# Optimization experiments

Hardware: AMD Instinct MI355X
Metric: run time of the kernel (lower is better)

## Reference

```python
import jax, jax.numpy as jnp
import numpy as np

N_NODES = 100000
N_EDGES = 1600000
IN_DIM = 128
HID = 32
HEADS = 4
OUT_DIM = 40
BN_EPS = 1e-5
NEG_SLOPE = 0.2


def _gat_conv(x, src, dst, W, att_src, att_dst, bias, concat):
    # x: [N, F_in]; src/dst: [E] (self-loops already appended)
    H, C = att_src.shape
    h = (x @ W).reshape(-1, H, C)                       # [N, H, C]
    a_s = jnp.sum(h * att_src, axis=-1)                 # [N, H]
    a_d = jnp.sum(h * att_dst, axis=-1)                 # [N, H]
    e = jax.nn.leaky_relu(a_s[src] + a_d[dst], NEG_SLOPE)  # [E, H]
    # segment softmax over incoming edges of each destination node
    m = jax.ops.segment_max(e, dst, num_segments=N_NODES)
    m = jnp.where(jnp.isfinite(m), m, 0.0)
    p = jnp.exp(e - m[dst])
    denom = jax.ops.segment_sum(p, dst, num_segments=N_NODES)
    alpha = p / (denom[dst] + 1e-16)                    # [E, H]
    out = jax.ops.segment_sum(h[src] * alpha[..., None], dst, num_segments=N_NODES)  # [N, H, C]
    out = out.reshape(N_NODES, H * C) if concat else out.mean(axis=1)
    return out + bias


def _bn_eval(x, gamma, beta, rm, rv):
    return (x - rm) * jax.lax.rsqrt(rv + BN_EPS) * gamma + beta


def setup_inputs() -> dict:
    key = jax.random.key(0)
    ks = jax.random.split(key, 16)
    d = {}
    d["x"] = jax.random.normal(ks[0], (N_NODES, IN_DIM), dtype=jnp.float32)
    d["edge_index"] = jax.random.randint(ks[1], (2, N_EDGES), 0, N_NODES, dtype=jnp.int64 if jax.config.jax_enable_x64 else jnp.int32)
    s = 0.1
    # conv1: IN_DIM -> HID x HEADS (concat)
    d["W1"] = jax.random.normal(ks[2], (IN_DIM, HEADS * HID), jnp.float32) * s
    d["as1"] = jax.random.normal(ks[3], (HEADS, HID), jnp.float32) * s
    d["ad1"] = jax.random.normal(ks[4], (HEADS, HID), jnp.float32) * s
    d["b1"] = jnp.zeros((HEADS * HID,), jnp.float32)
    d["g1"] = jnp.ones((HEADS * HID,), jnp.float32)
    d["beta1"] = jnp.zeros((HEADS * HID,), jnp.float32)
    d["rm1"] = jnp.zeros((HEADS * HID,), jnp.float32)
    d["rv1"] = jnp.ones((HEADS * HID,), jnp.float32)
    # conv2: HID*HEADS -> HID (1 head, no concat)
    d["W2"] = jax.random.normal(ks[5], (HEADS * HID, HID), jnp.float32) * s
    d["as2"] = jax.random.normal(ks[6], (1, HID), jnp.float32) * s
    d["ad2"] = jax.random.normal(ks[7], (1, HID), jnp.float32) * s
    d["b2"] = jnp.zeros((HID,), jnp.float32)
    d["g2"] = jnp.ones((HID,), jnp.float32)
    d["beta2"] = jnp.zeros((HID,), jnp.float32)
    d["rm2"] = jnp.zeros((HID,), jnp.float32)
    d["rv2"] = jnp.ones((HID,), jnp.float32)
    # conv3: HID -> OUT_DIM (1 head, no concat)
    d["W3"] = jax.random.normal(ks[8], (HID, OUT_DIM), jnp.float32) * s
    d["as3"] = jax.random.normal(ks[9], (1, OUT_DIM), jnp.float32) * s
    d["ad3"] = jax.random.normal(ks[10], (1, OUT_DIM), jnp.float32) * s
    d["b3"] = jnp.zeros((OUT_DIM,), jnp.float32)
    return d


def reference(x, edge_index, W1, as1, ad1, b1, g1, beta1, rm1, rv1,
              W2, as2, ad2, b2, g2, beta2, rm2, rv2, W3, as3, ad3, b3):
    # add self-loops (PyG GATConv default), shared by all three layers
    loops = jnp.arange(N_NODES, dtype=edge_index.dtype)
    src = jnp.concatenate([edge_index[0], loops])
    dst = jnp.concatenate([edge_index[1], loops])
    h = _gat_conv(x, src, dst, W1, as1, ad1, b1, concat=True)
    h = jax.nn.elu(_bn_eval(h, g1, beta1, rm1, rv1))
    h = _gat_conv(h, src, dst, W2, as2, ad2, b2, concat=False)
    h = jax.nn.elu(_bn_eval(h, g2, beta2, rm2, rv2))
    out = _gat_conv(h, src, dst, W3, as3, ad3, b3, concat=False)
    return jax.nn.log_softmax(out, axis=1)
```

## Files before the change

### kernel.cpp

```cpp
#include <hip/hip_runtime.h>
#include <math.h>

#define N_NODES 100000
#define N_EDGES 1600000
#define E_TOT   (N_EDGES + N_NODES)
#define BN_EPS  1e-5f
#define NEG_SLOPE 0.2f
#define NINF (-INFINITY)


__global__ __launch_bounds__(256) void k_count(const int* __restrict__ ei,
                                               int* __restrict__ cnt) {
    int i = blockIdx.x * blockDim.x + threadIdx.x;
    if (i >= E_TOT) return;
    int d = (i < N_EDGES) ? ei[N_EDGES + i] : (i - N_EDGES);
    atomicAdd(&cnt[d], 1);
}

__global__ __launch_bounds__(256) void k_scan1(const int* __restrict__ cnt,
                                               int* __restrict__ excl,
                                               int* __restrict__ sums) {
    __shared__ int lds[256];
    int t = threadIdx.x;
    int base = blockIdx.x * 1024 + t * 4;
    int a[4];
#pragma unroll
    for (int j = 0; j < 4; ++j) a[j] = (base + j < N_NODES) ? cnt[base + j] : 0;
    int tot = a[0] + a[1] + a[2] + a[3];
    lds[t] = tot;
    __syncthreads();
    for (int off = 1; off < 256; off <<= 1) {
        int v = (t >= off) ? lds[t - off] : 0;
        __syncthreads();
        lds[t] += v;
        __syncthreads();
    }
    int run = lds[t] - tot;
#pragma unroll
    for (int j = 0; j < 4; ++j) {
        if (base + j < N_NODES) excl[base + j] = run;
        run += a[j];
    }
    if (t == 255) sums[blockIdx.x] = lds[255];
}

__global__ void k_scan2(int* sums, int nb) {
    if (blockIdx.x == 0 && threadIdx.x == 0) {
        int run = 0;
        for (int i = 0; i < nb; ++i) { int v = sums[i]; sums[i] = run; run += v; }
    }
}

__global__ __launch_bounds__(256) void k_scan3(int* __restrict__ row_ptr,
                                               int* __restrict__ cursor,
                                               const int* __restrict__ sums) {
    int i = blockIdx.x * blockDim.x + threadIdx.x;
    if (i == 0) row_ptr[N_NODES] = E_TOT;
    if (i >= N_NODES) return;
    int v = row_ptr[i] + sums[i >> 10];
    row_ptr[i] = v;
    cursor[i] = v;
}

__global__ __launch_bounds__(256) void k_scatter(const int* __restrict__ ei,
                                                 int* __restrict__ cursor,
                                                 int* __restrict__ col_idx) {
    int i = blockIdx.x * blockDim.x + threadIdx.x;
    if (i >= E_TOT) return;
    int s, d;
    if (i < N_EDGES) { s = ei[i]; d = ei[N_EDGES + i]; }
    else             { s = d = i - N_EDGES; }
    int pos = atomicAdd(&cursor[d], 1);
    col_idx[pos] = s;
}


template <int K, int NC, int BM, int BLOCK>
__global__ __launch_bounds__(BLOCK) void k_gemm(const float* __restrict__ X,
                                                const float* __restrict__ W,
                                                float* __restrict__ Hout,
                                                int nrows) {
    constexpr int CG  = NC / 4;
    constexpr int TR  = BLOCK / CG;
    constexpr int RPT = BM / TR;
    constexpr int LDK = K + 4;
    __shared__ float xs[BM * LDK];
    const int row0 = blockIdx.x * BM;
    const int vr = (nrows - row0 < BM) ? (nrows - row0) : BM;
    const int nvalid = vr * K;
    for (int i = threadIdx.x * 4; i < BM * K; i += BLOCK * 4) {
        float4 v = make_float4(0.f, 0.f, 0.f, 0.f);
        if (i < nvalid) v = *(const float4*)(X + (size_t)row0 * K + i);
        int row = i / K, col = i % K;
        *(float4*)(&xs[row * LDK + col]) = v;
    }
    __syncthreads();
    const int tx = threadIdx.x % CG;
    const int ty = threadIdx.x / CG;
    float4 acc[RPT];
#pragma unroll
    for (int r = 0; r < RPT; ++r) acc[r] = make_float4(0.f, 0.f, 0.f, 0.f);
    for (int k4 = 0; k4 < K / 4; ++k4) {
        const float4 w0 = *(const float4*)(W + (k4 * 4 + 0) * NC + tx * 4);
        const float4 w1 = *(const float4*)(W + (k4 * 4 + 1) * NC + tx * 4);
        const float4 w2 = *(const float4*)(W + (k4 * 4 + 2) * NC + tx * 4);
        const float4 w3 = *(const float4*)(W + (k4 * 4 + 3) * NC + tx * 4);
#pragma unroll
        for (int r = 0; r < RPT; ++r) {
            const float4 xv = *(const float4*)(&xs[(ty * RPT + r) * LDK + k4 * 4]);
            acc[r].x = fmaf(xv.w, w3.x, fmaf(xv.z, w2.x, fmaf(xv.y, w1.x, fmaf(xv.x, w0.x, acc[r].x))));
            acc[r].y = fmaf(xv.w, w3.y, fmaf(xv.z, w2.y, fmaf(xv.y, w1.y, fmaf(xv.x, w0.y, acc[r].y))));
            acc[r].z = fmaf(xv.w, w3.z, fmaf(xv.z, w2.z, fmaf(xv.y, w1.z, fmaf(xv.x, w0.z, acc[r].z))));
            acc[r].w = fmaf(xv.w, w3.w, fmaf(xv.z, w2.w, fmaf(xv.y, w1.w, fmaf(xv.x, w0.w, acc[r].w))));
        }
    }
#pragma unroll
    for (int r = 0; r < RPT; ++r) {
        int row = row0 + ty * RPT + r;
        if (row < nrows) *(float4*)(Hout + (size_t)row * NC + tx * 4) = acc[r];
    }
}


__global__ __launch_bounds__(256) void k_attproj1(const float* __restrict__ h,
                                                  const float* __restrict__ asf,
                                                  const float* __restrict__ adf,
                                                  float* __restrict__ a_s,
                                                  float* __restrict__ a_d) {
    int wv = (blockIdx.x * blockDim.x + threadIdx.x) >> 6;
    int lane = threadIdx.x & 63;
    if (wv >= N_NODES) return;
    float hlo = h[(size_t)wv * 128 + lane];
    float hhi = h[(size_t)wv * 128 + 64 + lane];
    float s0 = hlo * asf[lane], s1 = hhi * asf[64 + lane];
    float d0 = hlo * adf[lane], d1 = hhi * adf[64 + lane];
#pragma unroll
    for (int off = 1; off < 32; off <<= 1) {
        s0 += __shfl_xor(s0, off); s1 += __shfl_xor(s1, off);
        d0 += __shfl_xor(d0, off); d1 += __shfl_xor(d1, off);
    }
    if (lane == 0)  { a_s[wv * 4 + 0] = s0; a_s[wv * 4 + 2] = s1;
                      a_d[wv * 4 + 0] = d0; a_d[wv * 4 + 2] = d1; }
    if (lane == 32) { a_s[wv * 4 + 1] = s0; a_s[wv * 4 + 3] = s1;
                      a_d[wv * 4 + 1] = d0; a_d[wv * 4 + 3] = d1; }
}

__global__ __launch_bounds__(256) void k_attproj2(const float* __restrict__ h,
                                                  const float* __restrict__ asf,
                                                  const float* __restrict__ adf,
                                                  float* __restrict__ a_s,
                                                  float* __restrict__ a_d) {
    int wv = (blockIdx.x * blockDim.x + threadIdx.x) >> 6;
    int lane = threadIdx.x & 63;
    if (wv * 2 >= N_NODES) return;
    int n = wv * 2 + (lane >> 5);
    int l = lane & 31;
    float hv = h[(size_t)n * 32 + l];
    float s = hv * asf[l], d = hv * adf[l];
#pragma unroll
    for (int off = 1; off < 32; off <<= 1) { s += __shfl_xor(s, off); d += __shfl_xor(d, off); }
    if (l == 0) { a_s[n] = s; a_d[n] = d; }
}

__global__ __launch_bounds__(256) void k_attproj3(const float* __restrict__ h,
                                                  const float* __restrict__ asf,
                                                  const float* __restrict__ adf,
                                                  float* __restrict__ a_s,
                                                  float* __restrict__ a_d) {
    int wv = (blockIdx.x * blockDim.x + threadIdx.x) >> 6;
    int lane = threadIdx.x & 63;
    if (wv >= N_NODES) return;
    float hv = (lane < 40) ? h[(size_t)wv * 40 + lane] : 0.f;
    float s = (lane < 40) ? hv * asf[lane] : 0.f;
    float d = (lane < 40) ? hv * adf[lane] : 0.f;
#pragma unroll
    for (int off = 1; off < 64; off <<= 1) { s += __shfl_xor(s, off); d += __shfl_xor(d, off); }
    if (lane == 0) { a_s[wv] = s; a_d[wv] = d; }
}


__global__ __launch_bounds__(256) void k_agg1(const float* __restrict__ h,
                                              const float* __restrict__ a_s,
                                              const float* __restrict__ a_d,
                                              const int* __restrict__ row_ptr,
                                              const int* __restrict__ col_idx,
                                              const float* __restrict__ b,
                                              const float* __restrict__ g,
                                              const float* __restrict__ beta,
                                              const float* __restrict__ rm,
                                              const float* __restrict__ rv,
                                              float* __restrict__ obuf) {
    __shared__ float4 lp[4 * 64];
    __shared__ int    lc[4 * 64];
    const int wid  = threadIdx.x >> 6;
    const int lane = threadIdx.x & 63;
    const int n = (blockIdx.x << 2) + wid;
    if (n >= N_NODES) return;
    float4* lpw = lp + (wid << 6);
    int*    lcw = lc + (wid << 6);
    const int hi = lane >> 5;
    const float4 ad4 = *(const float4*)(a_d + (size_t)n * 4);
    const int beg = row_ptr[n], end = row_ptr[n + 1];
    const int deg = end - beg;
    float den0 = 0.f, den1 = 0.f, den2 = 0.f, den3 = 0.f;
    float acc0 = 0.f, acc1 = 0.f;

    if (deg <= 64) {
        const int idx = beg + lane;
        const bool v = idx < end;
        const int col = v ? col_idx[idx] : 0;
        float e0, e1, e2, e3;
        if (v) {
            float4 as4 = *(const float4*)(a_s + (size_t)col * 4);
            e0 = as4.x + ad4.x; e0 = e0 > 0.f ? e0 : NEG_SLOPE * e0;
            e1 = as4.y + ad4.y; e1 = e1 > 0.f ? e1 : NEG_SLOPE * e1;
            e2 = as4.z + ad4.z; e2 = e2 > 0.f ? e2 : NEG_SLOPE * e2;
            e3 = as4.w + ad4.w; e3 = e3 > 0.f ? e3 : NEG_SLOPE * e3;
        } else { e0 = e1 = e2 = e3 = NINF; }
        float m0 = e0, m1 = e1, m2 = e2, m3 = e3;
#pragma unroll
        for (int off = 1; off < 64; off <<= 1) {
            m0 = fmaxf(m0, __shfl_xor(m0, off));
            m1 = fmaxf(m1, __shfl_xor(m1, off));
            m2 = fmaxf(m2, __shfl_xor(m2, off));
            m3 = fmaxf(m3, __shfl_xor(m3, off));
        }
        float p0 = __expf(e0 - m0), p1 = __expf(e1 - m1);
        float p2 = __expf(e2 - m2), p3 = __expf(e3 - m3);
        lpw[lane] = make_float4(p0, p1, p2, p3);
        lcw[lane] = col;
        den0 = p0; den1 = p1; den2 = p2; den3 = p3;
#pragma unroll
        for (int off = 1; off < 64; off <<= 1) {
            den0 += __shfl_xor(den0, off); den1 += __shfl_xor(den1, off);
            den2 += __shfl_xor(den2, off); den3 += __shfl_xor(den3, off);
        }
        const int cnt = (deg + 1) & ~1;
        for (int j = 0; j < cnt; j += 2) {
            float4 pa = lpw[j];
            float4 pb = lpw[j + 1];
            int c0 = lcw[j], c1 = lcw[j + 1];
            const float* r0 = h + (size_t)c0 * 128;
            const float* r1 = h + (size_t)c1 * 128;
            float h00 = r0[lane], h01 = r0[64 + lane];
            float h10 = r1[lane], h11 = r1[64 + lane];
            float pA0 = hi ? pa.y : pa.x, pB0 = hi ? pa.w : pa.z;
            float pA1 = hi ? pb.y : pb.x, pB1 = hi ? pb.w : pb.z;
            acc0 += pA0 * h00 + pA1 * h10;
            acc1 += pB0 * h01 + pB1 * h11;
        }
    } else {
        float m0 = NINF, m1 = NINF, m2 = NINF, m3 = NINF;
        for (int c = beg; c < end; c += 64) {
            int idx = c + lane;
            bool v = idx < end;
            if (v) {
                int col = col_idx[idx];
                float4 as4 = *(const float4*)(a_s + (size_t)col * 4);
                float e0 = as4.x + ad4.x; e0 = e0 > 0.f ? e0 : NEG_SLOPE * e0;
                float e1 = as4.y + ad4.y; e1 = e1 > 0.f ? e1 : NEG_SLOPE * e1;
                float e2 = as4.z + ad4.z; e2 = e2 > 0.f ? e2 : NEG_SLOPE * e2;
                float e3 = as4.w + ad4.w; e3 = e3 > 0.f ? e3 : NEG_SLOPE * e3;
                m0 = fmaxf(m0, e0); m1 = fmaxf(m1, e1);
                m2 = fmaxf(m2, e2); m3 = fmaxf(m3, e3);
            }
        }
#pragma unroll
        for (int off = 1; off < 64; off <<= 1) {
            m0 = fmaxf(m0, __shfl_xor(m0, off));
            m1 = fmaxf(m1, __shfl_xor(m1, off));
            m2 = fmaxf(m2, __shfl_xor(m2, off));
            m3 = fmaxf(m3, __shfl_xor(m3, off));
        }
        for (int c = beg; c < end; c += 64) {
            int idx = c + lane;
            bool v = idx < end;
            int col = v ? col_idx[idx] : 0;
            float p0 = 0.f, p1 = 0.f, p2 = 0.f, p3 = 0.f;
            if (v) {
                float4 as4 = *(const float4*)(a_s + (size_t)col * 4);
                float e0 = as4.x + ad4.x; e0 = e0 > 0.f ? e0 : NEG_SLOPE * e0;
                float e1 = as4.y + ad4.y; e1 = e1 > 0.f ? e1 : NEG_SLOPE * e1;
                float e2 = as4.z + ad4.z; e2 = e2 > 0.f ? e2 : NEG_SLOPE * e2;
                float e3 = as4.w + ad4.w; e3 = e3 > 0.f ? e3 : NEG_SLOPE * e3;
                p0 = __expf(e0 - m0); p1 = __expf(e1 - m1);
                p2 = __expf(e2 - m2); p3 = __expf(e3 - m3);
            }
            lpw[lane] = make_float4(p0, p1, p2, p3);
            lcw[lane] = col;
            float s0 = p0, s1 = p1, s2 = p2, s3 = p3;
#pragma unroll
            for (int off = 1; off < 64; off <<= 1) {
                s0 += __shfl_xor(s0, off); s1 += __shfl_xor(s1, off);
                s2 += __shfl_xor(s2, off); s3 += __shfl_xor(s3, off);
            }
            den0 += s0; den1 += s1; den2 += s2; den3 += s3;
            int csz = end - c; if (csz > 64) csz = 64;
            int cnt = (csz + 1) & ~1;
            for (int j = 0; j < cnt; j += 2) {
                float4 pa = lpw[j];
                float4 pb = lpw[j + 1];
                int c0i = lcw[j], c1i = lcw[j + 1];
                const float* r0 = h + (size_t)c0i * 128;
                const float* r1 = h + (size_t)c1i * 128;
                float h00 = r0[lane], h01 = r0[64 + lane];
                float h10 = r1[lane], h11 = r1[64 + lane];
                float pA0 = hi ? pa.y : pa.x, pB0 = hi ? pa.w : pa.z;
                float pA1 = hi ? pb.y : pb.x, pB1 = hi ? pb.w : pb.z;
                acc0 += pA0 * h00 + pA1 * h10;
                acc1 += pB0 * h01 + pB1 * h11;
            }
        }
    }

    float inv0 = 1.f / (den0 + 1e-16f), inv1 = 1.f / (den1 + 1e-16f);
    float inv2 = 1.f / (den2 + 1e-16f), inv3 = 1.f / (den3 + 1e-16f);
    float f0 = acc0 * (hi ? inv1 : inv0);
    float f1 = acc1 * (hi ? inv3 : inv2);
    int fA = lane, fB = lane + 64;
    f0 += b[fA]; f1 += b[fB];
    f0 = (f0 - rm[fA]) * rsqrtf(rv[fA] + BN_EPS) * g[fA] + beta[fA];
    f1 = (f1 - rm[fB]) * rsqrtf(rv[fB] + BN_EPS) * g[fB] + beta[fB];
    f0 = f0 > 0.f ? f0 : (__expf(f0) - 1.f);
    f1 = f1 > 0.f ? f1 : (__expf(f1) - 1.f);
    obuf[(size_t)n * 128 + fA] = f0;
    obuf[(size_t)n * 128 + fB] = f1;
}

__global__ __launch_bounds__(256) void k_agg2(const float* __restrict__ h,
                                              const float* __restrict__ a_s,
                                              const float* __restrict__ a_d,
                                              const int* __restrict__ row_ptr,
                                              const int* __restrict__ col_idx,
                                              const float* __restrict__ b,
                                              const float* __restrict__ g,
                                              const float* __restrict__ beta,
                                              const float* __restrict__ rm,
                                              const float* __restrict__ rv,
                                              float* __restrict__ obuf) {
    __shared__ float lp[4 * 64];
    __shared__ int   lc[4 * 64];
    const int wid  = threadIdx.x >> 6;
    const int lane = threadIdx.x & 63;
    const int n = (blockIdx.x << 2) + wid;
    if (n >= N_NODES) return;
    float* lpw = lp + (wid << 6);
    int*   lcw = lc + (wid << 6);
    const int l31 = lane & 31, hh = lane >> 5;
    const float ad = a_d[n];
    const int beg = row_ptr[n], end = row_ptr[n + 1];
    const int deg = end - beg;
    float den = 0.f, acc = 0.f;

    if (deg <= 64) {
        const int idx = beg + lane;
        const bool v = idx < end;
        const int col = v ? col_idx[idx] : 0;
        float e = NINF;
        if (v) {
            e = a_s[col] + ad;
            e = e > 0.f ? e : NEG_SLOPE * e;
        }
        float m = e;
#pragma unroll
        for (int off = 1; off < 64; off <<= 1) m = fmaxf(m, __shfl_xor(m, off));
        float p = __expf(e - m);
        lpw[lane] = p;
        lcw[lane] = col;
        den = p;
#pragma unroll
        for (int off = 1; off < 64; off <<= 1) den += __shfl_xor(den, off);
        const int cnt = (deg + 1) & ~1;
        for (int j = 0; j < cnt; j += 2) {
            int jj = j + hh;
            float p_ = lpw[jj];
            int c  = lcw[jj];
            acc += p_ * h[(size_t)c * 32 + l31];
        }
    } else {
        float m = NINF;
        for (int c = beg; c < end; c += 64) {
            int idx = c + lane;
            if (idx < end) {
                float e = a_s[col_idx[idx]] + ad;
                e = e > 0.f ? e : NEG_SLOPE * e;
                m = fmaxf(m, e);
            }
        }
#pragma unroll
        for (int off = 1; off < 64; off <<= 1) m = fmaxf(m, __shfl_xor(m, off));
        for (int c = beg; c < end; c += 64) {
            int idx = c + lane;
            bool v = idx < end;
            int col = v ? col_idx[idx] : 0;
            float p = 0.f;
            if (v) {
                float e = a_s[col] + ad;
                e = e > 0.f ? e : NEG_SLOPE * e;
                p = __expf(e - m);
            }
            lpw[lane] = p;
            lcw[lane] = col;
            float s = p;
#pragma unroll
            for (int off = 1; off < 64; off <<= 1) s += __shfl_xor(s, off);
            den += s;
            int csz = end - c; if (csz > 64) csz = 64;
            int cnt = (csz + 1) & ~1;
            for (int j = 0; j < cnt; j += 2) {
                int jj = j + hh;
                float p_ = lpw[jj];
                int cc = lcw[jj];
                acc += p_ * h[(size_t)cc * 32 + l31];
            }
        }
    }
    acc += __shfl_xor(acc, 32);
    float vout = acc / (den + 1e-16f);
    vout += b[l31];
    vout = (vout - rm[l31]) * rsqrtf(rv[l31] + BN_EPS) * g[l31] + beta[l31];
    vout = vout > 0.f ? vout : (__expf(vout) - 1.f);
    if (lane < 32) obuf[(size_t)n * 32 + lane] = vout;
}

__global__ __launch_bounds__(256) void k_agg3(const float* __restrict__ h,
                                              const float* __restrict__ a_s,
                                              const float* __restrict__ a_d,
                                              const int* __restrict__ row_ptr,
                                              const int* __restrict__ col_idx,
                                              const float* __restrict__ b,
                                              float* __restrict__ out) {
    __shared__ float lp[4 * 64];
    __shared__ int   lc[4 * 64];
    const int wid  = threadIdx.x >> 6;
    const int lane = threadIdx.x & 63;
    const int n = (blockIdx.x << 2) + wid;
    if (n >= N_NODES) return;
    float* lpw = lp + (wid << 6);
    int*   lcw = lc + (wid << 6);
    const float ad = a_d[n];
    const int beg = row_ptr[n], end = row_ptr[n + 1];
    const int deg = end - beg;
    float den = 0.f, acc = 0.f;

    if (deg <= 64) {
        const int idx = beg + lane;
        const bool v = idx < end;
        const int col = v ? col_idx[idx] : 0;
        float e = NINF;
        if (v) {
            e = a_s[col] + ad;
            e = e > 0.f ? e : NEG_SLOPE * e;
        }
        float m = e;
#pragma unroll
        for (int off = 1; off < 64; off <<= 1) m = fmaxf(m, __shfl_xor(m, off));
        float p = __expf(e - m);
        lpw[lane] = p;
        lcw[lane] = col;
        den = p;
#pragma unroll
        for (int off = 1; off < 64; off <<= 1) den += __shfl_xor(den, off);
        const int cnt = (deg + 1) & ~1;
        for (int j = 0; j < cnt; j += 2) {
            float p0 = lpw[j], p1 = lpw[j + 1];
            int c0 = lcw[j], c1 = lcw[j + 1];
            if (lane < 40) {
                acc += p0 * h[(size_t)c0 * 40 + lane] + p1 * h[(size_t)c1 * 40 + lane];
            }
        }
    } else {
        float m = NINF;
        for (int c = beg; c < end; c += 64) {
            int idx = c + lane;
            if (idx < end) {
                float e = a_s[col_idx[idx]] + ad;
                e = e > 0.f ? e : NEG_SLOPE * e;
                m = fmaxf(m, e);
            }
        }
#pragma unroll
        for (int off = 1; off < 64; off <<= 1) m = fmaxf(m, __shfl_xor(m, off));
        for (int c = beg; c < end; c += 64) {
            int idx = c + lane;
            bool v = idx < end;
            int col = v ? col_idx[idx] : 0;
            float p = 0.f;
            if (v) {
                float e = a_s[col] + ad;
                e = e > 0.f ? e : NEG_SLOPE * e;
                p = __expf(e - m);
            }
            lpw[lane] = p;
            lcw[lane] = col;
            float s = p;
#pragma unroll
            for (int off = 1; off < 64; off <<= 1) s += __shfl_xor(s, off);
            den += s;
            int csz = end - c; if (csz > 64) csz = 64;
            int cnt = (csz + 1) & ~1;
            for (int j = 0; j < cnt; j += 2) {
                float p0 = lpw[j], p1 = lpw[j + 1];
                int c0i = lcw[j], c1i = lcw[j + 1];
                if (lane < 40) {
                    acc += p0 * h[(size_t)c0i * 40 + lane] + p1 * h[(size_t)c1i * 40 + lane];
                }
            }
        }
    }
    float vv = acc / (den + 1e-16f) + b[lane < 40 ? lane : 0];
    float vm = (lane < 40) ? vv : NINF;
#pragma unroll
    for (int off = 1; off < 64; off <<= 1) vm = fmaxf(vm, __shfl_xor(vm, off));
    float ex = (lane < 40) ? __expf(vv - vm) : 0.f;
#pragma unroll
    for (int off = 1; off < 64; off <<= 1) ex += __shfl_xor(ex, off);
    float res = vv - vm - logf(ex);
    if (lane < 40) out[(size_t)n * 40 + lane] = res;
}


extern "C" void kernel_launch(void* const* d_in, const int* in_sizes, int n_in,
                              void* d_out, int out_size, void* d_ws, size_t ws_size,
                              hipStream_t stream) {
    const float* x    = (const float*)d_in[0];
    const int*   ei   = (const int*)d_in[1];
    const float* W1   = (const float*)d_in[2];
    const float* as1  = (const float*)d_in[3];
    const float* ad1  = (const float*)d_in[4];
    const float* b1   = (const float*)d_in[5];
    const float* g1   = (const float*)d_in[6];
    const float* be1  = (const float*)d_in[7];
    const float* rm1  = (const float*)d_in[8];
    const float* rv1  = (const float*)d_in[9];
    const float* W2   = (const float*)d_in[10];
    const float* as2  = (const float*)d_in[11];
    const float* ad2  = (const float*)d_in[12];
    const float* b2   = (const float*)d_in[13];
    const float* g2   = (const float*)d_in[14];
    const float* be2  = (const float*)d_in[15];
    const float* rm2  = (const float*)d_in[16];
    const float* rv2  = (const float*)d_in[17];
    const float* W3   = (const float*)d_in[18];
    const float* as3  = (const float*)d_in[19];
    const float* ad3  = (const float*)d_in[20];
    const float* b3   = (const float*)d_in[21];
    float* out = (float*)d_out;

    char* base = (char*)d_ws;
    size_t off = 0;
    auto carve = [&](size_t bytes) {
        char* p = base + off;
        off = (off + bytes + 255) & ~(size_t)255;
        return p;
    };
    int*   row_ptr = (int*)carve((N_NODES + 1) * sizeof(int));
    int*   cnt     = (int*)carve(N_NODES * sizeof(int));
    int*   cursor  = (int*)carve(N_NODES * sizeof(int));
    int*   sums    = (int*)carve(1024 * sizeof(int));
    int*   col_idx = (int*)carve((size_t)E_TOT * sizeof(int));
    float* a_s     = (float*)carve((size_t)N_NODES * 4 * sizeof(float));
    float* a_d     = (float*)carve((size_t)N_NODES * 4 * sizeof(float));
    float* hbuf    = (float*)carve((size_t)N_NODES * 128 * sizeof(float));
    float* obuf    = (float*)carve((size_t)N_NODES * 128 * sizeof(float));
    (void)ws_size;

    hipMemsetAsync(cnt, 0, N_NODES * sizeof(int), stream);
    {
        int g1b = (E_TOT + 255) / 256;
        k_count<<<g1b, 256, 0, stream>>>(ei, cnt);
        int nb = (N_NODES + 1023) / 1024;
        k_scan1<<<nb, 256, 0, stream>>>(cnt, row_ptr, sums);
        k_scan2<<<1, 1, 0, stream>>>(sums, nb);
        k_scan3<<<(N_NODES + 255) / 256, 256, 0, stream>>>(row_ptr, cursor, sums);
        k_scatter<<<g1b, 256, 0, stream>>>(ei, cursor, col_idx);
    }

    const int GEMM_GRID = (N_NODES + 63) / 64;
    const int WPN   = (N_NODES + 3) / 4;
    const int WP2N  = (N_NODES / 2 + 3) / 4;

    k_gemm<128, 128, 64, 256><<<GEMM_GRID, 256, 0, stream>>>(x, W1, hbuf, N_NODES);
    k_attproj1<<<WPN, 256, 0, stream>>>(hbuf, as1, ad1, a_s, a_d);
    k_agg1<<<WPN, 256, 0, stream>>>(hbuf, a_s, a_d, row_ptr, col_idx,
                                    b1, g1, be1, rm1, rv1, obuf);

    k_gemm<128, 32, 64, 256><<<GEMM_GRID, 256, 0, stream>>>(obuf, W2, hbuf, N_NODES);
    k_attproj2<<<WP2N, 256, 0, stream>>>(hbuf, as2, ad2, a_s, a_d);
    k_agg2<<<WPN, 256, 0, stream>>>(hbuf, a_s, a_d, row_ptr, col_idx,
                                    b2, g2, be2, rm2, rv2, obuf);

    k_gemm<32, 40, 64, 320><<<GEMM_GRID, 320, 0, stream>>>(obuf, W3, hbuf, N_NODES);
    k_attproj3<<<WPN, 256, 0, stream>>>(hbuf, as3, ad3, a_s, a_d);
    k_agg3<<<WPN, 256, 0, stream>>>(hbuf, a_s, a_d, row_ptr, col_idx, b3, out);
}
```

Baseline: 785.3 us.

## Fuse attention projections into GEMM epilogue and unroll gather loops by four

Layers 1 and 2 now compute the per-head attention scores a_s/a_d inside the GEMM epilogue using 8-lane shuffle reductions, which removes two separate attproj kernels and their re-read of the hidden matrix. The aggregation kernels of all three layers also unroll the neighbour gather loop from two to four rows per iteration, so more independent global loads are in flight. The cost is more registers and extra padded iterations on the LDS arrays for low-degree nodes.

Measured after the change: 714.8 us. 1.1x faster.

```diff
diff --git a/kernel.cpp b/kernel.cpp
--- a/kernel.cpp
+++ b/kernel.cpp
@@ -122,45 +122,74 @@
 }
 
 
-__global__ __launch_bounds__(256) void k_attproj1(const float* __restrict__ h,
-                                                  const float* __restrict__ asf,
-                                                  const float* __restrict__ adf,
-                                                  float* __restrict__ a_s,
-                                                  float* __restrict__ a_d) {
-    int wv = (blockIdx.x * blockDim.x + threadIdx.x) >> 6;
-    int lane = threadIdx.x & 63;
-    if (wv >= N_NODES) return;
-    float hlo = h[(size_t)wv * 128 + lane];
-    float hhi = h[(size_t)wv * 128 + 64 + lane];
-    float s0 = hlo * asf[lane], s1 = hhi * asf[64 + lane];
-    float d0 = hlo * adf[lane], d1 = hhi * adf[64 + lane];
-#pragma unroll
-    for (int off = 1; off < 32; off <<= 1) {
-        s0 += __shfl_xor(s0, off); s1 += __shfl_xor(s1, off);
-        d0 += __shfl_xor(d0, off); d1 += __shfl_xor(d1, off);
-    }
-    if (lane == 0)  { a_s[wv * 4 + 0] = s0; a_s[wv * 4 + 2] = s1;
-                      a_d[wv * 4 + 0] = d0; a_d[wv * 4 + 2] = d1; }
-    if (lane == 32) { a_s[wv * 4 + 1] = s0; a_s[wv * 4 + 3] = s1;
-                      a_d[wv * 4 + 1] = d0; a_d[wv * 4 + 3] = d1; }
-}
-
-__global__ __launch_bounds__(256) void k_attproj2(const float* __restrict__ h,
-                                                  const float* __restrict__ asf,
-                                                  const float* __restrict__ adf,
-                                                  float* __restrict__ a_s,
-                                                  float* __restrict__ a_d) {
-    int wv = (blockIdx.x * blockDim.x + threadIdx.x) >> 6;
-    int lane = threadIdx.x & 63;
-    if (wv * 2 >= N_NODES) return;
-    int n = wv * 2 + (lane >> 5);
-    int l = lane & 31;
-    float hv = h[(size_t)n * 32 + l];
-    float s = hv * asf[l], d = hv * adf[l];
-#pragma unroll
-    for (int off = 1; off < 32; off <<= 1) { s += __shfl_xor(s, off); d += __shfl_xor(d, off); }
-    if (l == 0) { a_s[n] = s; a_d[n] = d; }
-}
+template <int K, int NC, int BM, int BLOCK, int HEADS_>
+__global__ __launch_bounds__(BLOCK) void k_gemm_ap(const float* __restrict__ X,
+                                                   const float* __restrict__ W,
+                                                   const float* __restrict__ asf,
+                                                   const float* __restrict__ adf,
+                                                   float* __restrict__ a_s,
+                                                   float* __restrict__ a_d,
+                                                   float* __restrict__ Hout,
+                                                   int nrows) {
+    constexpr int CG  = NC / 4;
+    constexpr int TR  = BLOCK / CG;
+    constexpr int RPT = BM / TR;
+    constexpr int LDK = K + 4;
+    constexpr int GL  = NC / HEADS_ / 4;
+    static_assert(GL == 8, "epilogue assumes 8-lane groups");
+    __shared__ float xs[BM * LDK];
+    const int row0 = blockIdx.x * BM;
+    const int vr = (nrows - row0 < BM) ? (nrows - row0) : BM;
+    const int nvalid = vr * K;
+    for (int i = threadIdx.x * 4; i < BM * K; i += BLOCK * 4) {
+        float4 v = make_float4(0.f, 0.f, 0.f, 0.f);
+        if (i < nvalid) v = *(const float4*)(X + (size_t)row0 * K + i);
+        int row = i / K, col = i % K;
+        *(float4*)(&xs[row * LDK + col]) = v;
+    }
+    __syncthreads();
+    const int tx = threadIdx.x % CG;
+    const int ty = threadIdx.x / CG;
+    float4 acc[RPT];
+#pragma unroll
+    for (int r = 0; r < RPT; ++r) acc[r] = make_float4(0.f, 0.f, 0.f, 0.f);
+    for (int k4 = 0; k4 < K / 4; ++k4) {
+        const float4 w0 = *(const float4*)(W + (k4 * 4 + 0) * NC + tx * 4);
+        const float4 w1 = *(const float4*)(W + (k4 * 4 + 1) * NC + tx * 4);
+        const float4 w2 = *(const float4*)(W + (k4 * 4 + 2) * NC + tx * 4);
+        const float4 w3 = *(const float4*)(W + (k4 * 4 + 3) * NC + tx * 4);
+#pragma unroll
+        for (int r = 0; r < RPT; ++r) {
+            const float4 xv = *(const float4*)(&xs[(ty * RPT + r) * LDK + k4 * 4]);
+            acc[r].x = fmaf(xv.w, w3.x, fmaf(xv.z, w2.x, fmaf(xv.y, w1.x, fmaf(xv.x, w0.x, acc[r].x))));
+            acc[r].y = fmaf(xv.w, w3.y, fmaf(xv.z, w2.y, fmaf(xv.y, w1.y, fmaf(xv.x, w0.y, acc[r].y))));
+            acc[r].z = fmaf(xv.w, w3.z, fmaf(xv.z, w2.z, fmaf(xv.y, w1.z, fmaf(xv.x, w0.z, acc[r].z))));
+            acc[r].w = fmaf(xv.w, w3.w, fmaf(xv.z, w2.w, fmaf(xv.y, w1.w, fmaf(xv.x, w0.w, acc[r].w))));
+        }
+    }
+    const int head = tx >> 3;
+    const float4 asv = *(const float4*)(asf + tx * 4);
+    const float4 adv = *(const float4*)(adf + tx * 4);
+#pragma unroll
+    for (int r = 0; r < RPT; ++r) {
+        int row = row0 + ty * RPT + r;
+        float ps = acc[r].x * asv.x + acc[r].y * asv.y + acc[r].z * asv.z + acc[r].w * asv.w;
+        float pd = acc[r].x * adv.x + acc[r].y * adv.y + acc[r].z * adv.z + acc[r].w * adv.w;
+#pragma unroll
+        for (int off = 1; off < GL; off <<= 1) {
+            ps += __shfl_xor(ps, off);
+            pd += __shfl_xor(pd, off);
+        }
+        if (row < nrows) {
+            *(float4*)(Hout + (size_t)row * NC + tx * 4) = acc[r];
+            if ((tx & (GL - 1)) == 0) {
+                a_s[(size_t)row * HEADS_ + head] = ps;
+                a_d[(size_t)row * HEADS_ + head] = pd;
+            }
+        }
+    }
+}
+
 
 __global__ __launch_bounds__(256) void k_attproj3(const float* __restrict__ h,
                                                   const float* __restrict__ asf,
@@ -235,19 +264,25 @@
             den0 += __shfl_xor(den0, off); den1 += __shfl_xor(den1, off);
             den2 += __shfl_xor(den2, off); den3 += __shfl_xor(den3, off);
         }
-        const int cnt = (deg + 1) & ~1;
-        for (int j = 0; j < cnt; j += 2) {
-            float4 pa = lpw[j];
-            float4 pb = lpw[j + 1];
-            int c0 = lcw[j], c1 = lcw[j + 1];
+        const int cnt = (deg + 3) & ~3;
+        for (int j = 0; j < cnt; j += 4) {
+            float4 pa = lpw[j],     pb = lpw[j + 1];
+            float4 pc = lpw[j + 2], pq = lpw[j + 3];
+            int c0 = lcw[j], c1 = lcw[j + 1], c2 = lcw[j + 2], c3 = lcw[j + 3];
             const float* r0 = h + (size_t)c0 * 128;
             const float* r1 = h + (size_t)c1 * 128;
+            const float* r2 = h + (size_t)c2 * 128;
+            const float* r3 = h + (size_t)c3 * 128;
             float h00 = r0[lane], h01 = r0[64 + lane];
             float h10 = r1[lane], h11 = r1[64 + lane];
+            float h20 = r2[lane], h21 = r2[64 + lane];
+            float h30 = r3[lane], h31 = r3[64 + lane];
             float pA0 = hi ? pa.y : pa.x, pB0 = hi ? pa.w : pa.z;
             float pA1 = hi ? pb.y : pb.x, pB1 = hi ? pb.w : pb.z;
-            acc0 += pA0 * h00 + pA1 * h10;
-            acc1 += pB0 * h01 + pB1 * h11;
+            float pA2 = hi ? pc.y : pc.x, pB2 = hi ? pc.w : pc.z;
+            float pA3 = hi ? pq.y : pq.x, pB3 = hi ? pq.w : pq.z;
+            acc0 += pA0 * h00 + pA1 * h10 + pA2 * h20 + pA3 * h30;
+            acc1 += pB0 * h01 + pB1 * h11 + pB2 * h21 + pB3 * h31;
         }
     } else {
         float m0 = NINF, m1 = NINF, m2 = NINF, m3 = NINF;
@@ -296,19 +331,25 @@
             }
             den0 += s0; den1 += s1; den2 += s2; den3 += s3;
             int csz = end - c; if (csz > 64) csz = 64;
-            int cnt = (csz + 1) & ~1;
-            for (int j = 0; j < cnt; j += 2) {
-                float4 pa = lpw[j];
-                float4 pb = lpw[j + 1];
-                int c0i = lcw[j], c1i = lcw[j + 1];
+            int cnt = (csz + 3) & ~3;
+            for (int j = 0; j < cnt; j += 4) {
+                float4 pa = lpw[j],     pb = lpw[j + 1];
+                float4 pc = lpw[j + 2], pq = lpw[j + 3];
+                int c0i = lcw[j], c1i = lcw[j + 1], c2i = lcw[j + 2], c3i = lcw[j + 3];
                 const float* r0 = h + (size_t)c0i * 128;
                 const float* r1 = h + (size_t)c1i * 128;
+                const float* r2 = h + (size_t)c2i * 128;
+                const float* r3 = h + (size_t)c3i * 128;
                 float h00 = r0[lane], h01 = r0[64 + lane];
                 float h10 = r1[lane], h11 = r1[64 + lane];
+                float h20 = r2[lane], h21 = r2[64 + lane];
+                float h30 = r3[lane], h31 = r3[64 + lane];
                 float pA0 = hi ? pa.y : pa.x, pB0 = hi ? pa.w : pa.z;
                 float pA1 = hi ? pb.y : pb.x, pB1 = hi ? pb.w : pb.z;
-                acc0 += pA0 * h00 + pA1 * h10;
-                acc1 += pB0 * h01 + pB1 * h11;
+                float pA2 = hi ? pc.y : pc.x, pB2 = hi ? pc.w : pc.z;
+                float pA3 = hi ? pq.y : pq.x, pB3 = hi ? pq.w : pq.z;
+                acc0 += pA0 * h00 + pA1 * h10 + pA2 * h20 + pA3 * h30;
+                acc1 += pB0 * h01 + pB1 * h11 + pB2 * h21 + pB3 * h31;
             }
         }
     }
@@ -370,12 +411,13 @@
         den = p;
 #pragma unroll
         for (int off = 1; off < 64; off <<= 1) den += __shfl_xor(den, off);
-        const int cnt = (deg + 1) & ~1;
-        for (int j = 0; j < cnt; j += 2) {
-            int jj = j + hh;
-            float p_ = lpw[jj];
-            int c  = lcw[jj];
-            acc += p_ * h[(size_t)c * 32 + l31];
+        const int cnt = (deg + 7) & ~7;
+        for (int j = 0; j < cnt; j += 8) {
+            int j0 = j + (hh << 2);
+            float p0 = lpw[j0], p1 = lpw[j0 + 1], p2 = lpw[j0 + 2], p3 = lpw[j0 + 3];
+            int c0 = lcw[j0], c1 = lcw[j0 + 1], c2 = lcw[j0 + 2], c3 = lcw[j0 + 3];
+            acc += p0 * h[(size_t)c0 * 32 + l31] + p1 * h[(size_t)c1 * 32 + l31]
+                 + p2 * h[(size_t)c2 * 32 + l31] + p3 * h[(size_t)c3 * 32 + l31];
         }
     } else {
         float m = NINF;
@@ -406,12 +448,13 @@
             for (int off = 1; off < 64; off <<= 1) s += __shfl_xor(s, off);
             den += s;
             int csz = end - c; if (csz > 64) csz = 64;
-            int cnt = (csz + 1) & ~1;
-            for (int j = 0; j < cnt; j += 2) {
-                int jj = j + hh;
-                float p_ = lpw[jj];
-                int cc = lcw[jj];
-                acc += p_ * h[(size_t)cc * 32 + l31];
+            int cnt = (csz + 7) & ~7;
+            for (int j = 0; j < cnt; j += 8) {
+                int j0 = j + (hh << 2);
+                float p0 = lpw[j0], p1 = lpw[j0 + 1], p2 = lpw[j0 + 2], p3 = lpw[j0 + 3];
+                int c0 = lcw[j0], c1 = lcw[j0 + 1], c2 = lcw[j0 + 2], c3 = lcw[j0 + 3];
+                acc += p0 * h[(size_t)c0 * 32 + l31] + p1 * h[(size_t)c1 * 32 + l31]
+                     + p2 * h[(size_t)c2 * 32 + l31] + p3 * h[(size_t)c3 * 32 + l31];
             }
         }
     }
@@ -461,12 +504,13 @@
         den = p;
 #pragma unroll
         for (int off = 1; off < 64; off <<= 1) den += __shfl_xor(den, off);
-        const int cnt = (deg + 1) & ~1;
-        for (int j = 0; j < cnt; j += 2) {
-            float p0 = lpw[j], p1 = lpw[j + 1];
-            int c0 = lcw[j], c1 = lcw[j + 1];
+        const int cnt = (deg + 3) & ~3;
+        for (int j = 0; j < cnt; j += 4) {
+            float p0 = lpw[j], p1 = lpw[j + 1], p2 = lpw[j + 2], p3 = lpw[j + 3];
+            int c0 = lcw[j], c1 = lcw[j + 1], c2 = lcw[j + 2], c3 = lcw[j + 3];
             if (lane < 40) {
-                acc += p0 * h[(size_t)c0 * 40 + lane] + p1 * h[(size_t)c1 * 40 + lane];
+                acc += p0 * h[(size_t)c0 * 40 + lane] + p1 * h[(size_t)c1 * 40 + lane]
+                     + p2 * h[(size_t)c2 * 40 + lane] + p3 * h[(size_t)c3 * 40 + lane];
             }
         }
     } else {
@@ -498,12 +542,13 @@
             for (int off = 1; off < 64; off <<= 1) s += __shfl_xor(s, off);
             den += s;
             int csz = end - c; if (csz > 64) csz = 64;
-            int cnt = (csz + 1) & ~1;
-            for (int j = 0; j < cnt; j += 2) {
-                float p0 = lpw[j], p1 = lpw[j + 1];
-                int c0i = lcw[j], c1i = lcw[j + 1];
+            int cnt = (csz + 3) & ~3;
+            for (int j = 0; j < cnt; j += 4) {
+                float p0 = lpw[j], p1 = lpw[j + 1], p2 = lpw[j + 2], p3 = lpw[j + 3];
+                int c0 = lcw[j], c1 = lcw[j + 1], c2 = lcw[j + 2], c3 = lcw[j + 3];
                 if (lane < 40) {
-                    acc += p0 * h[(size_t)c0i * 40 + lane] + p1 * h[(size_t)c1i * 40 + lane];
+                    acc += p0 * h[(size_t)c0 * 40 + lane] + p1 * h[(size_t)c1 * 40 + lane]
+                         + p2 * h[(size_t)c2 * 40 + lane] + p3 * h[(size_t)c3 * 40 + lane];
                 }
             }
         }
@@ -577,16 +622,15 @@
     }
 
     const int GEMM_GRID = (N_NODES + 63) / 64;
-    const int WPN   = (N_NODES + 3) / 4;
-    const int WP2N  = (N_NODES / 2 + 3) / 4;
-
-    k_gemm<128, 128, 64, 256><<<GEMM_GRID, 256, 0, stream>>>(x, W1, hbuf, N_NODES);
-    k_attproj1<<<WPN, 256, 0, stream>>>(hbuf, as1, ad1, a_s, a_d);
+    const int WPN = (N_NODES + 3) / 4;
+
+    k_gemm_ap<128, 128, 64, 256, 4><<<GEMM_GRID, 256, 0, stream>>>(
+        x, W1, as1, ad1, a_s, a_d, hbuf, N_NODES);
     k_agg1<<<WPN, 256, 0, stream>>>(hbuf, a_s, a_d, row_ptr, col_idx,
                                     b1, g1, be1, rm1, rv1, obuf);
 
-    k_gemm<128, 32, 64, 256><<<GEMM_GRID, 256, 0, stream>>>(obuf, W2, hbuf, N_NODES);
-    k_attproj2<<<WP2N, 256, 0, stream>>>(hbuf, as2, ad2, a_s, a_d);
+    k_gemm_ap<128, 32, 64, 256, 1><<<GEMM_GRID, 256, 0, stream>>>(
+        obuf, W2, as2, ad2, a_s, a_d, hbuf, N_NODES);
     k_agg2<<<WPN, 256, 0, stream>>>(hbuf, a_s, a_d, row_ptr, col_idx,
                                     b2, g2, be2, rm2, rv2, obuf);
 
```
